# Performance work log

Measured on AMD Instinct MI355X. Metric: run time of the kernel, lower is better.

The kernel has to match this reference:

```python
import jax, jax.numpy as jnp
import numpy as np

DIM = 768
H = 16
HD = DIM // H  # 48


def setup_inputs() -> dict:
    key = jax.random.key(0)
    ks = jax.random.split(key, 9)
    s = 0.02
    return {
        "x": jax.random.normal(ks[0], (8, 1024, DIM), dtype=jnp.float32),
        "w_qkv": jax.random.normal(ks[1], (3 * DIM, DIM), dtype=jnp.float32) * s,
        "b_qkv": jax.random.normal(ks[2], (3 * DIM,), dtype=jnp.float32) * s,
        "w_l": jax.random.normal(ks[3], (H, H), dtype=jnp.float32) * 0.25,
        "b_l": jax.random.normal(ks[4], (H,), dtype=jnp.float32) * s,
        "w_w": jax.random.normal(ks[5], (H, H), dtype=jnp.float32) * 0.25,
        "b_w": jax.random.normal(ks[6], (H,), dtype=jnp.float32) * s,
        "w_proj": jax.random.normal(ks[7], (DIM, DIM), dtype=jnp.float32) * s,
        "b_proj": jax.random.normal(ks[8], (DIM,), dtype=jnp.float32) * s,
    }


def reference(x, w_qkv, b_qkv, w_l, b_l, w_w, b_w, w_proj, b_proj):
    B, N, C = x.shape
    scale = HD ** -0.5
    qkv = x @ w_qkv.T + b_qkv                        # [B,N,3C]
    qkv = qkv.reshape(B, N, 3, H, HD).transpose(2, 0, 3, 1, 4)  # [3,B,H,N,HD]
    q = qkv[0] * scale
    k = qkv[1]
    v = qkv[2]
    attn = jnp.einsum('bhqd,bhkd->bhqk', q, k)       # [B,H,N,N]
    # talking-heads mix before softmax (Linear over head dim)
    attn = jnp.einsum('bhqk,gh->bgqk', attn, w_l) + b_l[None, :, None, None]
    attn = jax.nn.softmax(attn, axis=-1)
    # talking-heads mix after softmax
    attn = jnp.einsum('bhqk,gh->bgqk', attn, w_w) + b_w[None, :, None, None]
    out = jnp.einsum('bhqk,bhkd->bhqd', attn, v)     # [B,H,N,HD]
    out = out.transpose(0, 2, 1, 3).reshape(B, N, C)
    return out @ w_proj.T + b_proj
```

## Files before the change

kernel.cpp:

```cpp
#include <hip/hip_runtime.h>

typedef unsigned short u16;
typedef unsigned int u32;
using short8 = __attribute__((__ext_vector_type__(8))) short;
using f32x4  = __attribute__((__ext_vector_type__(4))) float;

#define DIM 768
#define QKV3 2304
#define SEQ 1024
#define SCALE 0.14433756729740643f

__device__ __forceinline__ u16 f2bf(float f) {
  __bf16 h = (__bf16)f;
  u16 r;
  __builtin_memcpy(&r, &h, 2);
  return r;
}
__device__ __forceinline__ u32 packbf(float lo, float hi) {
  return (u32)f2bf(lo) | ((u32)f2bf(hi) << 16);
}
__device__ __forceinline__ void store1(u16* p, float v) { *p = f2bf(v); }
__device__ __forceinline__ void store1(float* p, float v) { *p = v; }

__device__ __forceinline__ f32x4 mfma16(short8 a, short8 b, f32x4 c) {
  return __builtin_amdgcn_mfma_f32_16x16x32_bf16(a, b, c, 0, 0, 0);
}

__global__ __launch_bounds__(256)
void cvt_f32_bf16(const float* __restrict__ src, u16* __restrict__ dst, int n8) {
  int i = blockIdx.x * 256 + threadIdx.x;
  if (i < n8) {
    float4 a = ((const float4*)src)[2 * i];
    float4 b = ((const float4*)src)[2 * i + 1];
    uint4 o = {packbf(a.x, a.y), packbf(a.z, a.w), packbf(b.x, b.y), packbf(b.z, b.w)};
    ((uint4*)dst)[i] = o;
  }
}

template <typename TO>
__global__ __launch_bounds__(256, 2)
void gemm_mfma(const u16* __restrict__ A, const float* __restrict__ W,
               const float* __restrict__ bias, TO* __restrict__ C,
               int M, int N, int K) {
  __shared__ __align__(16) u16 As[128 * 40];
  __shared__ __align__(16) u16 Bs[128 * 40];
  const int tid = threadIdx.x;
  const int lane = tid & 63;
  const int wv = tid >> 6;
  const int lq = lane & 15;
  const int lc = lane >> 4;
  const int wm = wv >> 1, wn = wv & 1;
  const int row0 = blockIdx.y * 128, col0 = blockIdx.x * 128;

  f32x4 acc[4][4];
#pragma unroll
  for (int i = 0; i < 4; ++i)
#pragma unroll
    for (int j = 0; j < 4; ++j) acc[i][j] = (f32x4){0.f, 0.f, 0.f, 0.f};

  short8 pa[2];
  float4 pw[2][2];
  auto issue = [&](int k0) {
#pragma unroll
    for (int t = 0; t < 2; ++t) {
      int id = t * 256 + tid;
      int r = id >> 2, kc = (id & 3) * 8;
      pa[t] = *(const short8*)(A + (size_t)(row0 + r) * K + k0 + kc);
      const float* wp = W + (size_t)(col0 + r) * K + k0 + kc;
      pw[t][0] = *(const float4*)wp;
      pw[t][1] = *(const float4*)(wp + 4);
    }
  };

  issue(0);
#pragma unroll 1
  for (int k0 = 0; k0 < K; k0 += 32) {
    __syncthreads();
#pragma unroll
    for (int t = 0; t < 2; ++t) {
      int id = t * 256 + tid;
      int r = id >> 2, kc = (id & 3) * 8;
      *(short8*)(As + r * 40 + kc) = pa[t];
      uint4 wq = {packbf(pw[t][0].x, pw[t][0].y), packbf(pw[t][0].z, pw[t][0].w),
                  packbf(pw[t][1].x, pw[t][1].y), packbf(pw[t][1].z, pw[t][1].w)};
      *(uint4*)(Bs + r * 40 + kc) = wq;
    }
    if (k0 + 32 < K) issue(k0 + 32);
    __syncthreads();
    short8 af[4], bf8[4];
#pragma unroll
    for (int i = 0; i < 4; ++i)
      af[i] = *(const short8*)(As + (wm * 64 + i * 16 + lq) * 40 + lc * 8);
#pragma unroll
    for (int j = 0; j < 4; ++j)
      bf8[j] = *(const short8*)(Bs + (wn * 64 + j * 16 + lq) * 40 + lc * 8);
#pragma unroll
    for (int i = 0; i < 4; ++i)
#pragma unroll
      for (int j = 0; j < 4; ++j)
        acc[i][j] = mfma16(af[i], bf8[j], acc[i][j]);
  }
#pragma unroll
  for (int j = 0; j < 4; ++j) {
    int col = col0 + wn * 64 + j * 16 + lq;
    float bv = bias[col];
#pragma unroll
    for (int i = 0; i < 4; ++i)
#pragma unroll
      for (int r = 0; r < 4; ++r) {
        int row = row0 + wm * 64 + i * 16 + lc * 4 + r;
        store1(C + (size_t)row * N + col, acc[i][j][r] + bv);
      }
  }
}

#define KS_ELEMS 24848
#define ATTN_SMEM 160832

__global__ __launch_bounds__(512, 2)
void attn_kernel(const u16* __restrict__ qkv,
                 const float* __restrict__ wl, const float* __restrict__ bl,
                 const float* __restrict__ ww, const float* __restrict__ bw,
                 u16* __restrict__ obuf) {
  extern __shared__ __align__(16) u16 smem[];
  u16* const Ks = smem;
  u16* const Sb = smem + KS_ELEMS;
  u16* const Vs = smem + 2 * KS_ELEMS;

  const int tid = threadIdx.x;
  const int wv = tid >> 6;
  const int lane = tid & 63;
  const int lq = lane & 15;
  const int lc = lane >> 4;
  const int b = blockIdx.x >> 5;
  const int qt = blockIdx.x & 31;
  const size_t tokQ = (size_t)b * SEQ + (size_t)qt * 32;
  const size_t tokB = (size_t)b * SEQ;
  const int h0 = wv * 2;

  {
    u32* z = (u32*)smem;
    for (int i = tid; i < KS_ELEMS; i += 512) z[i] = 0u;
  }

  short8 qf[2][2][2];
#pragma unroll
  for (int hh = 0; hh < 2; ++hh)
#pragma unroll
    for (int qs = 0; qs < 2; ++qs) {
      const u16* qp = qkv + (tokQ + qs * 16 + lq) * QKV3 + (h0 + hh) * 48;
      qf[hh][qs][0] = *(const short8*)(qp + lc * 8);
      short8 z8 = {0, 0, 0, 0, 0, 0, 0, 0};
      if (lc < 2) z8 = *(const short8*)(qp + 32 + lc * 8);
      qf[hh][qs][1] = z8;
    }

  short8 wlF = {0, 0, 0, 0, 0, 0, 0, 0};
  short8 wwF = {0, 0, 0, 0, 0, 0, 0, 0};
  if (lc < 2) {
#pragma unroll
    for (int e = 0; e < 8; ++e) {
      wlF[e] = (short)f2bf(wl[lq * 16 + lc * 8 + e] * SCALE);
      wwF[e] = (short)f2bf(ww[lq * 16 + lc * 8 + e]);
    }
  }
  float blr[4], bwr[4];
#pragma unroll
  for (int r = 0; r < 4; ++r) { blr[r] = bl[lc * 4 + r]; bwr[r] = bw[lc * 4 + r]; }

  short8 kpre[6], vA[3], vB[3];
  auto issueK = [&](int kt) {
#pragma unroll
    for (int t = 0; t < 6; ++t) {
      int j = t * 512 + tid;
      int kr = j / 96, cc = j - kr * 96;
      kpre[t] = *(const short8*)(qkv + (tokB + (size_t)kt * 32 + kr) * QKV3 + DIM + cc * 8);
    }
  };
  auto issueV = [&](int kt) {
#pragma unroll
    for (int t = 0; t < 3; ++t) {
      int cc = (tid >> 4) + t * 32;
      int kk = tid & 15;
      const u16* v0 = qkv + (tokB + (size_t)kt * 32 + 2 * kk) * QKV3 + 2 * DIM + cc * 8;
      vA[t] = *(const short8*)v0;
      vB[t] = *(const short8*)(v0 + QKV3);
    }
  };
  auto writeK = [&]() {
#pragma unroll
    for (int t = 0; t < 6; ++t) {
      int j = t * 512 + tid;
      int kr = j / 96, cc = j - kr * 96;
      *(short8*)(Ks + kr * 776 + cc * 8) = kpre[t];
    }
  };
  auto writeV = [&]() {
#pragma unroll
    for (int t = 0; t < 3; ++t) {
      int cc = (tid >> 4) + t * 32;
      int kk = tid & 15;
#pragma unroll
      for (int e = 0; e < 8; ++e)
        *(u32*)(Vs + (cc * 8 + e) * 40 + 2 * kk) =
            (u32)(u16)vA[t][e] | ((u32)(u16)vB[t][e] << 16);
    }
  };
  auto doQK = [&]() {
#pragma unroll
    for (int ks = 0; ks < 2; ++ks) {
      short8 kf[2][2];
#pragma unroll
      for (int hh = 0; hh < 2; ++hh) {
        const u16* kb = Ks + (ks * 16 + lq) * 776 + (h0 + hh) * 48;
        kf[hh][0] = *(const short8*)(kb + lc * 8);
        kf[hh][1] = *(const short8*)(kb + 32 + lc * 8);
      }
#pragma unroll
      for (int qs = 0; qs < 2; ++qs) {
        f32x4 s0 = {0.f, 0.f, 0.f, 0.f}, s1 = {0.f, 0.f, 0.f, 0.f};
        s0 = mfma16(qf[0][qs][0], kf[0][0], s0);
        s0 = mfma16(qf[0][qs][1], kf[0][1], s0);
        s1 = mfma16(qf[1][qs][0], kf[1][0], s1);
        s1 = mfma16(qf[1][qs][1], kf[1][1], s1);
#pragma unroll
        for (int r = 0; r < 4; ++r) {
          int q = qs * 16 + lc * 4 + r;
          int k = ks * 16 + lq;
          *(u32*)(Sb + q * 776 + k * 24 + h0) = packbf(s0[r], s1[r]);
        }
      }
    }
  };

  float Zac[4][4], invZ[4][4];
#pragma unroll
  for (int i = 0; i < 4; ++i)
#pragma unroll
    for (int r = 0; r < 4; ++r) Zac[i][r] = 0.f;

  f32x4 O[2][3][2];
#pragma unroll
  for (int hh = 0; hh < 2; ++hh)
#pragma unroll
    for (int dt = 0; dt < 3; ++dt)
#pragma unroll
      for (int qs = 0; qs < 2; ++qs) O[hh][dt][qs] = (f32x4){0.f, 0.f, 0.f, 0.f};

  issueK(0);
#pragma unroll 1
  for (int kt = 0; kt < 32; ++kt) {
    __syncthreads();
    writeK();
    if (kt + 1 < 32) issueK(kt + 1);
    else { issueK(0); issueV(0); }
    __syncthreads();
    doQK();
    __syncthreads();
#pragma unroll
    for (int i = 0; i < 4; ++i) {
      const int q = wv * 4 + i;
      const u16* sq = Sb + q * 776;
#pragma unroll
      for (int ks = 0; ks < 2; ++ks) {
        short8 sf = *(const short8*)(sq + (ks * 16 + lq) * 24 + lc * 8);
        f32x4 cin = {blr[0], blr[1], blr[2], blr[3]};
        f32x4 L = mfma16(wlF, sf, cin);
#pragma unroll
        for (int r = 0; r < 4; ++r) Zac[i][r] += __expf(L[r]);
      }
    }
  }
#pragma unroll
  for (int i = 0; i < 4; ++i)
#pragma unroll
    for (int r = 0; r < 4; ++r) {
      float z = Zac[i][r];
      z += __shfl_xor(z, 1);
      z += __shfl_xor(z, 2);
      z += __shfl_xor(z, 4);
      z += __shfl_xor(z, 8);
      invZ[i][r] = 1.0f / z;
    }

#pragma unroll 1
  for (int kt = 0; kt < 32; ++kt) {
    __syncthreads();
    writeK();
    writeV();
    if (kt + 1 < 32) { issueK(kt + 1); issueV(kt + 1); }
    __syncthreads();
    doQK();
    __syncthreads();
#pragma unroll
    for (int i = 0; i < 4; ++i) {
      const int q = wv * 4 + i;
      u16* const sq = Sb + q * 776;
      f32x4 L[2];
#pragma unroll
      for (int ks = 0; ks < 2; ++ks) {
        short8 sf = *(const short8*)(sq + (ks * 16 + lq) * 24 + lc * 8);
        f32x4 cin = {blr[0], blr[1], blr[2], blr[3]};
        L[ks] = mfma16(wlF, sf, cin);
      }
#pragma unroll
      for (int ks = 0; ks < 2; ++ks) {
        float p0 = __expf(L[ks][0]) * invZ[i][0];
        float p1 = __expf(L[ks][1]) * invZ[i][1];
        float p2 = __expf(L[ks][2]) * invZ[i][2];
        float p3 = __expf(L[ks][3]) * invZ[i][3];
        u16* pp = sq + (ks * 16 + lq) * 24 + lc * 4;
        *(u32*)pp = packbf(p0, p1);
        *(u32*)(pp + 2) = packbf(p2, p3);
      }
      f32x4 W2[2];
#pragma unroll
      for (int ks = 0; ks < 2; ++ks) {
        short8 pf = *(const short8*)(sq + (ks * 16 + lq) * 24 + lc * 8);
        f32x4 cin = {bwr[0], bwr[1], bwr[2], bwr[3]};
        W2[ks] = mfma16(wwF, pf, cin);
      }
#pragma unroll
      for (int ks = 0; ks < 2; ++ks)
#pragma unroll
        for (int r = 0; r < 4; ++r)
          sq[(lc * 4 + r) * 40 + ks * 16 + lq] = f2bf(W2[ks][r]);
    }
    __syncthreads();
#pragma unroll
    for (int hh = 0; hh < 2; ++hh) {
      const int g2 = h0 + hh;
      short8 w2f[2];
#pragma unroll
      for (int qs = 0; qs < 2; ++qs)
        w2f[qs] = *(const short8*)(Sb + (qs * 16 + lq) * 776 + g2 * 40 + lc * 8);
#pragma unroll
      for (int dt = 0; dt < 3; ++dt) {
        short8 vf = *(const short8*)(Vs + (g2 * 48 + dt * 16 + lq) * 40 + lc * 8);
#pragma unroll
        for (int qs = 0; qs < 2; ++qs)
          O[hh][dt][qs] = mfma16(w2f[qs], vf, O[hh][dt][qs]);
      }
    }
  }

#pragma unroll
  for (int hh = 0; hh < 2; ++hh)
#pragma unroll
    for (int dt = 0; dt < 3; ++dt)
#pragma unroll
      for (int qs = 0; qs < 2; ++qs)
#pragma unroll
        for (int r = 0; r < 4; ++r) {
          size_t row = tokQ + qs * 16 + lc * 4 + r;
          int col = (h0 + hh) * 48 + dt * 16 + lq;
          obuf[row * DIM + col] = f2bf(O[hh][dt][qs][r]);
        }
}

extern "C" void kernel_launch(void* const* d_in, const int* in_sizes, int n_in,
                              void* d_out, int out_size, void* d_ws, size_t ws_size,
                              hipStream_t stream) {
  const float* x      = (const float*)d_in[0];
  const float* w_qkv  = (const float*)d_in[1];
  const float* b_qkv  = (const float*)d_in[2];
  const float* w_l    = (const float*)d_in[3];
  const float* b_l    = (const float*)d_in[4];
  const float* w_w    = (const float*)d_in[5];
  const float* b_w    = (const float*)d_in[6];
  const float* w_proj = (const float*)d_in[7];
  const float* b_proj = (const float*)d_in[8];
  float* out = (float*)d_out;

  u16* qkv_buf  = (u16*)d_ws;
  u16* attn_buf = qkv_buf + (size_t)8192 * QKV3;
  u16* x_bf     = attn_buf;

  static int attr_done = 0;
  if (!attr_done) {
    (void)hipFuncSetAttribute(reinterpret_cast<const void*>(attn_kernel),
                              hipFuncAttributeMaxDynamicSharedMemorySize,
                              ATTN_SMEM);
    attr_done = 1;
  }

  cvt_f32_bf16<<<dim3(786432 / 256), 256, 0, stream>>>(x, x_bf, 786432);
  gemm_mfma<u16><<<dim3(QKV3 / 128, 8192 / 128), 256, 0, stream>>>(
      x_bf, w_qkv, b_qkv, qkv_buf, 8192, QKV3, DIM);
  attn_kernel<<<dim3(8 * 32), dim3(512), ATTN_SMEM, stream>>>(
      qkv_buf, w_l, b_l, w_w, b_w, attn_buf);
  gemm_mfma<float><<<dim3(DIM / 128, 8192 / 128), 256, 0, stream>>>(
      attn_buf, w_proj, b_proj, out, 8192, DIM, DIM);
}
```

Before: 360.0 us.

## Load K fragments directly from global into registers, drop K shared-memory staging

```diff
diff --git a/kernel.cpp b/kernel.cpp
--- a/kernel.cpp
+++ b/kernel.cpp
@@ -114,8 +114,8 @@
   }
 }
 
-#define KS_ELEMS 24848
-#define ATTN_SMEM 160832
+#define SB_ELEMS 24848
+#define ATTN_SMEM 111136
 
 __global__ __launch_bounds__(512, 2)
 void attn_kernel(const u16* __restrict__ qkv,
@@ -123,9 +123,8 @@
                  const float* __restrict__ ww, const float* __restrict__ bw,
                  u16* __restrict__ obuf) {
   extern __shared__ __align__(16) u16 smem[];
-  u16* const Ks = smem;
-  u16* const Sb = smem + KS_ELEMS;
-  u16* const Vs = smem + 2 * KS_ELEMS;
+  u16* const Sb = smem;
+  u16* const Vs = smem + SB_ELEMS;
 
   const int tid = threadIdx.x;
   const int wv = tid >> 6;
@@ -140,7 +139,7 @@
 
   {
     u32* z = (u32*)smem;
-    for (int i = tid; i < KS_ELEMS; i += 512) z[i] = 0u;
+    for (int i = tid; i < SB_ELEMS / 2; i += 512) z[i] = 0u;
   }
 
   short8 qf[2][2][2];
@@ -168,15 +167,8 @@
 #pragma unroll
   for (int r = 0; r < 4; ++r) { blr[r] = bl[lc * 4 + r]; bwr[r] = bw[lc * 4 + r]; }
 
-  short8 kpre[6], vA[3], vB[3];
-  auto issueK = [&](int kt) {
-#pragma unroll
-    for (int t = 0; t < 6; ++t) {
-      int j = t * 512 + tid;
-      int kr = j / 96, cc = j - kr * 96;
-      kpre[t] = *(const short8*)(qkv + (tokB + (size_t)kt * 32 + kr) * QKV3 + DIM + cc * 8);
-    }
-  };
+  short8 vA[3], vB[3];
+  short8 kf[2][2][2];
   auto issueV = [&](int kt) {
 #pragma unroll
     for (int t = 0; t < 3; ++t) {
@@ -187,13 +179,16 @@
       vB[t] = *(const short8*)(v0 + QKV3);
     }
   };
-  auto writeK = [&]() {
-#pragma unroll
-    for (int t = 0; t < 6; ++t) {
-      int j = t * 512 + tid;
-      int kr = j / 96, cc = j - kr * 96;
-      *(short8*)(Ks + kr * 776 + cc * 8) = kpre[t];
-    }
+  auto issueKf = [&](int kt) {
+#pragma unroll
+    for (int ks = 0; ks < 2; ++ks)
+#pragma unroll
+      for (int hh = 0; hh < 2; ++hh) {
+        const u16* kb = qkv + (tokB + (size_t)kt * 32 + ks * 16 + lq) * QKV3 + DIM +
+                        (h0 + hh) * 48;
+        kf[ks][hh][0] = *(const short8*)(kb + lc * 8);
+        kf[ks][hh][1] = *(const short8*)(kb + 32 + lc * 8);
+      }
   };
   auto writeV = [&]() {
 #pragma unroll
@@ -208,21 +203,14 @@
   };
   auto doQK = [&]() {
 #pragma unroll
-    for (int ks = 0; ks < 2; ++ks) {
-      short8 kf[2][2];
-#pragma unroll
-      for (int hh = 0; hh < 2; ++hh) {
-        const u16* kb = Ks + (ks * 16 + lq) * 776 + (h0 + hh) * 48;
-        kf[hh][0] = *(const short8*)(kb + lc * 8);
-        kf[hh][1] = *(const short8*)(kb + 32 + lc * 8);
-      }
+    for (int ks = 0; ks < 2; ++ks)
 #pragma unroll
       for (int qs = 0; qs < 2; ++qs) {
         f32x4 s0 = {0.f, 0.f, 0.f, 0.f}, s1 = {0.f, 0.f, 0.f, 0.f};
-        s0 = mfma16(qf[0][qs][0], kf[0][0], s0);
-        s0 = mfma16(qf[0][qs][1], kf[0][1], s0);
-        s1 = mfma16(qf[1][qs][0], kf[1][0], s1);
-        s1 = mfma16(qf[1][qs][1], kf[1][1], s1);
+        s0 = mfma16(qf[0][qs][0], kf[ks][0][0], s0);
+        s0 = mfma16(qf[0][qs][1], kf[ks][0][1], s0);
+        s1 = mfma16(qf[1][qs][0], kf[ks][1][0], s1);
+        s1 = mfma16(qf[1][qs][1], kf[ks][1][1], s1);
 #pragma unroll
         for (int r = 0; r < 4; ++r) {
           int q = qs * 16 + lc * 4 + r;
@@ -230,7 +218,6 @@
           *(u32*)(Sb + q * 776 + k * 24 + h0) = packbf(s0[r], s1[r]);
         }
       }
-    }
   };
 
   float Zac[4][4], invZ[4][4];
@@ -247,15 +234,12 @@
 #pragma unroll
       for (int qs = 0; qs < 2; ++qs) O[hh][dt][qs] = (f32x4){0.f, 0.f, 0.f, 0.f};
 
-  issueK(0);
+  issueKf(0);
+  __syncthreads();
 #pragma unroll 1
   for (int kt = 0; kt < 32; ++kt) {
-    __syncthreads();
-    writeK();
-    if (kt + 1 < 32) issueK(kt + 1);
-    else { issueK(0); issueV(0); }
-    __syncthreads();
     doQK();
+    issueKf(kt + 1 < 32 ? kt + 1 : 0);
     __syncthreads();
 #pragma unroll
     for (int i = 0; i < 4; ++i) {
@@ -270,7 +254,9 @@
         for (int r = 0; r < 4; ++r) Zac[i][r] += __expf(L[r]);
       }
     }
-  }
+    __syncthreads();
+  }
+  issueV(0);
 #pragma unroll
   for (int i = 0; i < 4; ++i)
 #pragma unroll
@@ -285,12 +271,10 @@
 
 #pragma unroll 1
   for (int kt = 0; kt < 32; ++kt) {
-    __syncthreads();
-    writeK();
     writeV();
-    if (kt + 1 < 32) { issueK(kt + 1); issueV(kt + 1); }
-    __syncthreads();
+    issueV(kt + 1 < 32 ? kt + 1 : 0);
     doQK();
+    issueKf(kt + 1 < 32 ? kt + 1 : 0);
     __syncthreads();
 #pragma unroll
     for (int i = 0; i < 4; ++i) {
@@ -342,6 +326,7 @@
           O[hh][dt][qs] = mfma16(w2f[qs], vf, O[hh][dt][qs]);
       }
     }
+    __syncthreads();
   }
 
 #pragma unroll
```

Result: slower. 395.0 us (+9.7%).

## Pre-convert weights to bf16 and double-buffer K tiles in attention passes

Applied to the files above, without the earlier changes.

```diff
diff --git a/kernel.cpp b/kernel.cpp
--- a/kernel.cpp
+++ b/kernel.cpp
@@ -39,9 +39,9 @@
 
 template <typename TO>
 __global__ __launch_bounds__(256, 2)
-void gemm_mfma(const u16* __restrict__ A, const float* __restrict__ W,
-               const float* __restrict__ bias, TO* __restrict__ C,
-               int M, int N, int K) {
+void gemm_bb(const u16* __restrict__ A, const u16* __restrict__ W,
+             const float* __restrict__ bias, TO* __restrict__ C,
+             int M, int N, int K) {
   __shared__ __align__(16) u16 As[128 * 40];
   __shared__ __align__(16) u16 Bs[128 * 40];
   const int tid = threadIdx.x;
@@ -58,17 +58,14 @@
 #pragma unroll
     for (int j = 0; j < 4; ++j) acc[i][j] = (f32x4){0.f, 0.f, 0.f, 0.f};
 
-  short8 pa[2];
-  float4 pw[2][2];
+  short8 pa[2], pw[2];
   auto issue = [&](int k0) {
 #pragma unroll
     for (int t = 0; t < 2; ++t) {
       int id = t * 256 + tid;
       int r = id >> 2, kc = (id & 3) * 8;
       pa[t] = *(const short8*)(A + (size_t)(row0 + r) * K + k0 + kc);
-      const float* wp = W + (size_t)(col0 + r) * K + k0 + kc;
-      pw[t][0] = *(const float4*)wp;
-      pw[t][1] = *(const float4*)(wp + 4);
+      pw[t] = *(const short8*)(W + (size_t)(col0 + r) * K + k0 + kc);
     }
   };
 
@@ -81,9 +78,7 @@
       int id = t * 256 + tid;
       int r = id >> 2, kc = (id & 3) * 8;
       *(short8*)(As + r * 40 + kc) = pa[t];
-      uint4 wq = {packbf(pw[t][0].x, pw[t][0].y), packbf(pw[t][0].z, pw[t][0].w),
-                  packbf(pw[t][1].x, pw[t][1].y), packbf(pw[t][1].z, pw[t][1].w)};
-      *(uint4*)(Bs + r * 40 + kc) = wq;
+      *(short8*)(Bs + r * 40 + kc) = pw[t];
     }
     if (k0 + 32 < K) issue(k0 + 32);
     __syncthreads();
@@ -115,6 +110,7 @@
 }
 
 #define KS_ELEMS 24848
+#define SMEM_ELEMS 80416
 #define ATTN_SMEM 160832
 
 __global__ __launch_bounds__(512, 2)
@@ -123,9 +119,9 @@
                  const float* __restrict__ ww, const float* __restrict__ bw,
                  u16* __restrict__ obuf) {
   extern __shared__ __align__(16) u16 smem[];
-  u16* const Ks = smem;
-  u16* const Sb = smem + KS_ELEMS;
-  u16* const Vs = smem + 2 * KS_ELEMS;
+  u16* const Ks0 = smem;
+  u16* const Sb  = smem + KS_ELEMS;
+  u16* const Vs  = smem + 2 * KS_ELEMS;
 
   const int tid = threadIdx.x;
   const int wv = tid >> 6;
@@ -140,7 +136,7 @@
 
   {
     u32* z = (u32*)smem;
-    for (int i = tid; i < KS_ELEMS; i += 512) z[i] = 0u;
+    for (int i = tid; i < SMEM_ELEMS / 2; i += 512) z[i] = 0u;
   }
 
   short8 qf[2][2][2];
@@ -187,12 +183,12 @@
       vB[t] = *(const short8*)(v0 + QKV3);
     }
   };
-  auto writeK = [&]() {
+  auto writeK = [&](u16* dst) {
 #pragma unroll
     for (int t = 0; t < 6; ++t) {
       int j = t * 512 + tid;
       int kr = j / 96, cc = j - kr * 96;
-      *(short8*)(Ks + kr * 776 + cc * 8) = kpre[t];
+      *(short8*)(dst + kr * 776 + cc * 8) = kpre[t];
     }
   };
   auto writeV = [&]() {
@@ -206,13 +202,13 @@
             (u32)(u16)vA[t][e] | ((u32)(u16)vB[t][e] << 16);
     }
   };
-  auto doQK = [&]() {
+  auto doQK = [&](const u16* kbase) {
 #pragma unroll
     for (int ks = 0; ks < 2; ++ks) {
       short8 kf[2][2];
 #pragma unroll
       for (int hh = 0; hh < 2; ++hh) {
-        const u16* kb = Ks + (ks * 16 + lq) * 776 + (h0 + hh) * 48;
+        const u16* kb = kbase + (ks * 16 + lq) * 776 + (h0 + hh) * 48;
         kf[hh][0] = *(const short8*)(kb + lc * 8);
         kf[hh][1] = *(const short8*)(kb + 32 + lc * 8);
       }
@@ -232,6 +228,23 @@
       }
     }
   };
+  auto doPV = [&](f32x4 O[2][3][2]) {
+#pragma unroll
+    for (int hh = 0; hh < 2; ++hh) {
+      const int g2 = h0 + hh;
+      short8 w2f[2];
+#pragma unroll
+      for (int qs = 0; qs < 2; ++qs)
+        w2f[qs] = *(const short8*)(Sb + (qs * 16 + lq) * 776 + g2 * 40 + lc * 8);
+#pragma unroll
+      for (int dt = 0; dt < 3; ++dt) {
+        short8 vf = *(const short8*)(Vs + (g2 * 48 + dt * 16 + lq) * 40 + lc * 8);
+#pragma unroll
+        for (int qs = 0; qs < 2; ++qs)
+          O[hh][dt][qs] = mfma16(w2f[qs], vf, O[hh][dt][qs]);
+      }
+    }
+  };
 
   float Zac[4][4], invZ[4][4];
 #pragma unroll
@@ -248,14 +261,19 @@
       for (int qs = 0; qs < 2; ++qs) O[hh][dt][qs] = (f32x4){0.f, 0.f, 0.f, 0.f};
 
   issueK(0);
+  __syncthreads();
+  writeK(Ks0);
+  issueK(1);
+  __syncthreads();
 #pragma unroll 1
   for (int kt = 0; kt < 32; ++kt) {
-    __syncthreads();
-    writeK();
-    if (kt + 1 < 32) issueK(kt + 1);
-    else { issueK(0); issueV(0); }
-    __syncthreads();
-    doQK();
+    u16* cur = (kt & 1) ? Vs : Ks0;
+    u16* nxt = (kt & 1) ? Ks0 : Vs;
+    if (kt < 31) {
+      writeK(nxt);
+      issueK(kt == 30 ? 0 : kt + 2);
+    }
+    doQK(cur);
     __syncthreads();
 #pragma unroll
     for (int i = 0; i < 4; ++i) {
@@ -270,7 +288,9 @@
         for (int r = 0; r < 4; ++r) Zac[i][r] += __expf(L[r]);
       }
     }
-  }
+    __syncthreads();
+  }
+  issueV(0);
 #pragma unroll
   for (int i = 0; i < 4; ++i)
 #pragma unroll
@@ -285,12 +305,12 @@
 
 #pragma unroll 1
   for (int kt = 0; kt < 32; ++kt) {
-    __syncthreads();
-    writeK();
+    if (kt) doPV(O);
+    writeK(Ks0);
+    __syncthreads();
     writeV();
-    if (kt + 1 < 32) { issueK(kt + 1); issueV(kt + 1); }
-    __syncthreads();
-    doQK();
+    doQK(Ks0);
+    if (kt < 31) { issueK(kt + 1); issueV(kt + 1); }
     __syncthreads();
 #pragma unroll
     for (int i = 0; i < 4; ++i) {
@@ -327,22 +347,8 @@
           sq[(lc * 4 + r) * 40 + ks * 16 + lq] = f2bf(W2[ks][r]);
     }
     __syncthreads();
-#pragma unroll
-    for (int hh = 0; hh < 2; ++hh) {
-      const int g2 = h0 + hh;
-      short8 w2f[2];
-#pragma unroll
-      for (int qs = 0; qs < 2; ++qs)
-        w2f[qs] = *(const short8*)(Sb + (qs * 16 + lq) * 776 + g2 * 40 + lc * 8);
-#pragma unroll
-      for (int dt = 0; dt < 3; ++dt) {
-        short8 vf = *(const short8*)(Vs + (g2 * 48 + dt * 16 + lq) * 40 + lc * 8);
-#pragma unroll
-        for (int qs = 0; qs < 2; ++qs)
-          O[hh][dt][qs] = mfma16(w2f[qs], vf, O[hh][dt][qs]);
-      }
-    }
-  }
+  }
+  doPV(O);
 
 #pragma unroll
   for (int hh = 0; hh < 2; ++hh)
@@ -375,6 +381,8 @@
   u16* qkv_buf  = (u16*)d_ws;
   u16* attn_buf = qkv_buf + (size_t)8192 * QKV3;
   u16* x_bf     = attn_buf;
+  u16* w_qkv_bf  = (u16*)d_out;
+  u16* w_proj_bf = qkv_buf;
 
   static int attr_done = 0;
   if (!attr_done) {
@@ -384,11 +392,13 @@
     attr_done = 1;
   }
 
-  cvt_f32_bf16<<<dim3(786432 / 256), 256, 0, stream>>>(x, x_bf, 786432);
-  gemm_mfma<u16><<<dim3(QKV3 / 128, 8192 / 128), 256, 0, stream>>>(
-      x_bf, w_qkv, b_qkv, qkv_buf, 8192, QKV3, DIM);
+  cvt_f32_bf16<<<dim3(864), 256, 0, stream>>>(w_qkv, w_qkv_bf, 221184);
+  cvt_f32_bf16<<<dim3(3072), 256, 0, stream>>>(x, x_bf, 786432);
+  gemm_bb<u16><<<dim3(QKV3 / 128, 8192 / 128), 256, 0, stream>>>(
+      x_bf, w_qkv_bf, b_qkv, qkv_buf, 8192, QKV3, DIM);
   attn_kernel<<<dim3(8 * 32), dim3(512), ATTN_SMEM, stream>>>(
       qkv_buf, w_l, b_l, w_w, b_w, attn_buf);
-  gemm_mfma<float><<<dim3(DIM / 128, 8192 / 128), 256, 0, stream>>>(
-      attn_buf, w_proj, b_proj, out, 8192, DIM, DIM);
-}
+  cvt_f32_bf16<<<dim3(288), 256, 0, stream>>>(w_proj, w_proj_bf, 73728);
+  gemm_bb<float><<<dim3(DIM / 128, 8192 / 128), 256, 0, stream>>>(
+      attn_buf, w_proj_bf, b_proj, out, 8192, DIM, DIM);
+}
```

New measurement: 358.1 us. About the same (-0.5%).
